# Performance work log

Measured on AMD Instinct MI355X. Metric: run time of the kernel, lower is better.

The kernel has to match this reference:

```python
import jax, jax.numpy as jnp
import numpy as np

TEMPERATURE = 0.07
EPS = 1e-8


def setup_inputs() -> dict:
    key = jax.random.key(0)
    k1, k2 = jax.random.split(key)
    B, D = 8192, 256
    embeddings = jax.random.normal(k1, (B, D), dtype=jnp.float32)
    labels = jax.random.randint(k2, (B,), 0, 6, dtype=jnp.int64)
    return {"embeddings": embeddings, "labels": labels}


def reference(embeddings, labels):
    B = embeddings.shape[0]
    # F.normalize(p=2, dim=1): x / max(||x||, eps)
    norm = jnp.linalg.norm(embeddings, axis=1, keepdims=True)
    en = embeddings / jnp.maximum(norm, 1e-12)
    sim = en @ en.T  # [B, B]
    s = sim / TEMPERATURE

    eye = jnp.eye(B, dtype=bool)
    same = labels[:, None] == labels[None, :]
    pos_mask = same & ~eye            # [B, B]
    neg_mask = (~same) & ~eye         # [B, B]

    exp_s = jnp.exp(s)
    # per-row sum of exp over negatives (matches inner-loop denominator term)
    neg_sum = jnp.sum(jnp.where(neg_mask, exp_s, 0.0), axis=1)  # [B]

    # rows contribute only if they have >=1 positive AND >=1 negative
    row_valid = (pos_mask.sum(axis=1) > 0) & (neg_mask.sum(axis=1) > 0)
    pair_mask = pos_mask & row_valid[:, None]

    # -log( exp(s_ij) / (exp(s_ij) + neg_sum_i + 1e-8) ) per positive pair
    per_pair = -jnp.log(exp_s / (exp_s + neg_sum[:, None] + EPS))
    total = jnp.sum(jnp.where(pair_mask, per_pair, 0.0))
    count = jnp.sum(pair_mask)
    loss = jnp.where(count > 0, total / jnp.maximum(count, 1).astype(total.dtype), 0.0)
    return loss
```

## Files before the change

### kernel.cpp

```cpp
#include <hip/hip_runtime.h>
#include <hip/hip_bf16.h>

#define B_ 8192
#define D_ 256
#define TINV 14.285714285714285f
#define EPS_ 1e-8f
#define BK 32
#define NBLK 32
#define NT 64
#define NTRI (NT*(NT+1)/2)

typedef short short8 __attribute__((ext_vector_type(8)));
typedef float f32x4 __attribute__((ext_vector_type(4)));

__device__ __forceinline__ void mfma_bf16(f32x4& acc, short8 a, short8 b) {
    asm("v_mfma_f32_16x16x32_bf16 %0, %1, %2, %0" : "+v"(acc) : "v"(a), "v"(b));
}

__device__ __forceinline__ void mfma_fence() {
    __builtin_amdgcn_sched_barrier(0);
    asm volatile("s_nop 7\ns_nop 7" ::);
}

__device__ __forceinline__ unsigned short f2bf(float x) {
    __hip_bfloat16 h = __float2bfloat16(x);
    return __builtin_bit_cast(unsigned short, h);
}

__device__ __forceinline__ void tri_decode(int idx, int& bi, int& bj) {
    int t = NTRI - 1 - idx;
    int u = (int)((sqrtf(8.f * (float)t + 1.f) - 1.f) * 0.5f);
    while (u * (u + 1) / 2 > t) --u;
    while ((u + 1) * (u + 2) / 2 <= t) ++u;
    bi = (NT - 1) - u;
    bj = (NT - 1) - (t - u * (u + 1) / 2);
}

__device__ __forceinline__ void stage(const char* gbase, int row0, int k0,
                                      short* ldst, int lane, int wid) {
#pragma unroll
    for (int it = 0; it < 2; ++it) {
        int c = (wid << 1) + it;
        int p = (c << 6) + lane;
        int row = p >> 2;
        int kb = (p & 3) ^ ((row >> 1) & 3);
        const char* g = gbase + ((size_t)(row0 + row) * (D_ * 2) + (size_t)(k0 + kb * 8) * 2);
        __builtin_amdgcn_global_load_lds(
            (const __attribute__((address_space(1))) unsigned int*)g,
            (__attribute__((address_space(3))) unsigned int*)(ldst + (size_t)c * 512),
            16, 0, 0);
    }
}

__device__ __forceinline__ void compute_step(const short* lA, const short* lB,
                                             int lane, int wm, int wn, f32x4 acc[4][4]) {
    int rl = lane & 15, kb = lane >> 4;
    short8 a[4], b[4];
#pragma unroll
    for (int m = 0; m < 4; ++m) {
        int row = wm * 64 + m * 16 + rl;
        a[m] = ((const short8*)lA)[row * 4 + (kb ^ ((row >> 1) & 3))];
    }
#pragma unroll
    for (int n = 0; n < 4; ++n) {
        int row = wn * 64 + n * 16 + rl;
        b[n] = ((const short8*)lB)[row * 4 + (kb ^ ((row >> 1) & 3))];
    }
#pragma unroll
    for (int m = 0; m < 4; ++m)
#pragma unroll
        for (int n = 0; n < 4; ++n)
            mfma_bf16(acc[m][n], a[m], b[n]);
}

__device__ __forceinline__ void gemm_pipe(const char* enb, int i0, int j0,
                                          short (*lA)[128 * BK], short (*lB)[128 * BK],
                                          int lane, int wid, int wm, int wn,
                                          f32x4 acc[4][4]) {
    stage(enb, i0, 0, lA[0], lane, wid);
    stage(enb, j0, 0, lB[0], lane, wid);
#define PIPE_STEP(T, WAITS)                                                     \
    {                                                                           \
        if ((T) < 7) {                                                          \
            stage(enb, i0, ((T) + 1) * BK, lA[((T) + 1) & 1], lane, wid);       \
            stage(enb, j0, ((T) + 1) * BK, lB[((T) + 1) & 1], lane, wid);       \
        }                                                                       \
        asm volatile(WAITS ::: "memory");                                       \
        __builtin_amdgcn_sched_barrier(0);                                      \
        __builtin_amdgcn_s_barrier();                                           \
        __builtin_amdgcn_sched_barrier(0);                                      \
        compute_step(lA[(T) & 1], lB[(T) & 1], lane, wm, wn, acc);              \
        asm volatile("s_waitcnt lgkmcnt(0)" ::: "memory");                      \
        __builtin_amdgcn_sched_barrier(0);                                      \
        __builtin_amdgcn_s_barrier();                                           \
        __builtin_amdgcn_sched_barrier(0);                                      \
    }
    PIPE_STEP(0, "s_waitcnt vmcnt(4)")
    PIPE_STEP(1, "s_waitcnt vmcnt(4)")
    PIPE_STEP(2, "s_waitcnt vmcnt(4)")
    PIPE_STEP(3, "s_waitcnt vmcnt(4)")
    PIPE_STEP(4, "s_waitcnt vmcnt(4)")
    PIPE_STEP(5, "s_waitcnt vmcnt(4)")
    PIPE_STEP(6, "s_waitcnt vmcnt(4)")
    PIPE_STEP(7, "s_waitcnt vmcnt(0)")
#undef PIPE_STEP
    mfma_fence();
}

__global__ __launch_bounds__(256) void k_bhist(const int* __restrict__ labels,
                                               unsigned* __restrict__ blockhist,
                                               float* __restrict__ negsum,
                                               float* __restrict__ total) {
    __shared__ unsigned h[8];
    int b = blockIdx.x, t = threadIdx.x;
    if (t < 8) h[t] = 0;
    negsum[b * 256 + t] = 0.f;
    if (b == 0 && t == 0) *total = 0.f;
    __syncthreads();
    atomicAdd(&h[labels[b * 256 + t] & 7], 1u);
    __syncthreads();
    if (t < 8) blockhist[b * 8 + t] = h[t];
}

__global__ __launch_bounds__(256) void k_pos(const int* __restrict__ labels,
                                             const unsigned* __restrict__ blockhist,
                                             unsigned* __restrict__ hist,
                                             int* __restrict__ pos) {
    __shared__ unsigned cnt[8][NBLK];
    __shared__ unsigned clsbase[8];
    __shared__ unsigned wcnt[4][8];
    int b = blockIdx.x, t = threadIdx.x;
    { int bb = t >> 3, c = t & 7; cnt[c][bb] = blockhist[bb * 8 + c]; }
    __syncthreads();
    if (t < 8) {
        unsigned run = 0;
        for (int b2 = 0; b2 < NBLK; ++b2) {
            unsigned v = cnt[t][b2];
            cnt[t][b2] = run;
            run += v;
        }
        clsbase[t] = run;
        if (b == 0) hist[t] = run;
    }
    __syncthreads();
    if (t == 0) {
        unsigned run = 0;
        for (int c = 0; c < 8; ++c) {
            unsigned tot = clsbase[c];
            clsbase[c] = run;
            run += tot;
        }
    }
    __syncthreads();
    int row = b * 256 + t;
    int c = labels[row] & 7;
    int lane = t & 63, w = t >> 6;
    unsigned long long lanebelow = (1ull << lane) - 1ull;
    unsigned myrank = 0;
#pragma unroll
    for (int cv = 0; cv < 8; ++cv) {
        unsigned long long mask = __ballot(c == cv);
        if (lane == 0) wcnt[w][cv] = (unsigned)__popcll(mask);
        if (c == cv) myrank = (unsigned)__popcll(mask & lanebelow);
    }
    __syncthreads();
    unsigned pre = 0;
    for (int wp = 0; wp < 4; ++wp) if (wp < w) pre += wcnt[wp][c];
    pos[row] = (int)(clsbase[c] + cnt[c][b] + pre + myrank);
}

__global__ __launch_bounds__(256) void k_scatter(const float* __restrict__ emb,
                                                 const int* __restrict__ labels,
                                                 const int* __restrict__ pos,
                                                 __hip_bfloat16* __restrict__ en_s,
                                                 int* __restrict__ lab_s) {
    int row = blockIdx.x * 4 + (threadIdx.x >> 6);
    int lane = threadIdx.x & 63;
    float4 v = reinterpret_cast<const float4*>(emb)[(size_t)row * 64 + lane];
    float ss = v.x * v.x + v.y * v.y + v.z * v.z + v.w * v.w;
#pragma unroll
    for (int off = 32; off >= 1; off >>= 1) ss += __shfl_xor(ss, off, 64);
    float scale = 1.0f / fmaxf(sqrtf(ss), 1e-12f);
    int p = pos[row];
    ushort4 o;
    o.x = f2bf(v.x * scale);
    o.y = f2bf(v.y * scale);
    o.z = f2bf(v.z * scale);
    o.w = f2bf(v.w * scale);
    reinterpret_cast<ushort4*>(en_s)[(size_t)p * 64 + lane] = o;
    if (lane == 0) lab_s[p] = labels[row] & 7;
}

template <bool USEP>
__global__ __launch_bounds__(256) void k_negsum(const __hip_bfloat16* __restrict__ en,
                                                const int* __restrict__ lab_s,
                                                float* __restrict__ P,
                                                float* __restrict__ negsum) {
    __shared__ short lA[2][128 * BK];
    __shared__ short lB[2][128 * BK];
    __shared__ int sLi[128], sLj[128];
    int bi, bj;
    tri_decode(blockIdx.x, bi, bj);
    int i0 = bi * 128, j0 = bj * 128;
    int tid = threadIdx.x;
    if (tid < 128) sLi[tid] = lab_s[i0 + tid];
    else           sLj[tid - 128] = lab_s[j0 + tid - 128];
    __syncthreads();

    int lane = tid & 63, wid = tid >> 6;
    int wm = wid >> 1, wn = wid & 1;
    f32x4 acc[4][4] = {};
    gemm_pipe((const char*)en, i0, j0, lA, lB, lane, wid, wm, wn, acc);

    int rl = lane & 15, rowg = (lane >> 4) * 4;
    int lj[4], li[4][4];
#pragma unroll
    for (int n = 0; n < 4; ++n) lj[n] = sLj[wn * 64 + n * 16 + rl];
#pragma unroll
    for (int m = 0; m < 4; ++m)
#pragma unroll
        for (int r = 0; r < 4; ++r) li[m][r] = sLi[wm * 64 + m * 16 + rowg + r];

#pragma unroll
    for (int m = 0; m < 4; ++m)
#pragma unroll
        for (int n = 0; n < 4; ++n)
#pragma unroll
            for (int r = 0; r < 4; ++r)
                acc[m][n][r] = (li[m][r] != lj[n]) ? __expf(acc[m][n][r] * TINV) : 0.f;

    float* sredR = (float*)lA;
    float* sredC = (float*)lB;

#pragma unroll
    for (int m = 0; m < 4; ++m) {
        float part[4];
#pragma unroll
        for (int r = 0; r < 4; ++r)
            part[r] = acc[m][0][r] + acc[m][1][r] + acc[m][2][r] + acc[m][3][r];
#pragma unroll
        for (int off = 1; off < 16; off <<= 1)
#pragma unroll
            for (int r = 0; r < 4; ++r) part[r] += __shfl_xor(part[r], off, 64);
        if (rl == 0) {
#pragma unroll
            for (int r = 0; r < 4; ++r) {
                int row = wm * 64 + m * 16 + rowg + r;
                if (USEP) sredR[wn * 128 + row] = part[r];
                else      atomicAdd(&negsum[i0 + row], part[r]);
            }
        }
    }
    if (bi != bj) {
#pragma unroll
        for (int n = 0; n < 4; ++n) {
            float cp = 0.f;
#pragma unroll
            for (int m = 0; m < 4; ++m)
#pragma unroll
                for (int r = 0; r < 4; ++r) cp += acc[m][n][r];
            cp += __shfl_xor(cp, 16, 64);
            cp += __shfl_xor(cp, 32, 64);
            if (lane < 16) {
                int col = wn * 64 + n * 16 + rl;
                if (USEP) sredC[wm * 128 + col] = cp;
                else      atomicAdd(&negsum[j0 + col], cp);
            }
        }
    }
    if (USEP) {
        __syncthreads();
        if (tid < 128)
            P[(size_t)bj * B_ + i0 + tid] = sredR[tid] + sredR[128 + tid];
        else if (bi != bj)
            P[(size_t)bi * B_ + j0 + (tid - 128)] = sredC[tid - 128] + sredC[128 + (tid - 128)];
    }
}

__global__ __launch_bounds__(256) void k_red(const float* __restrict__ P,
                                             float* __restrict__ negsum) {
    int i = blockIdx.x * 256 + threadIdx.x;
    float s = 0.f;
#pragma unroll 8
    for (int k = 0; k < 64; ++k) s += P[(size_t)k * B_ + i];
    negsum[i] = s;
}

__global__ __launch_bounds__(256) void k_pairs(const __hip_bfloat16* __restrict__ en,
                                               const int* __restrict__ lab_s,
                                               const float* __restrict__ negsum,
                                               const unsigned* __restrict__ hist,
                                               float* __restrict__ total) {
    int bi, bj;
    tri_decode(blockIdx.x, bi, bj);
    int i0 = bi * 128, j0 = bj * 128;
    if (lab_s[j0] > lab_s[i0 + 127]) return;

    __shared__ short lA[2][128 * BK];
    __shared__ short lB[2][128 * BK];
    __shared__ int sLi[128], sLj[128];
    __shared__ float sNgI[128], sNgJ[128];
    int tid = threadIdx.x;
    if (tid < 128) {
        int l = lab_s[i0 + tid];
        unsigned h = hist[l];
        sLi[tid] = (h > 1u && h < (unsigned)B_) ? l : -1;
        sNgI[tid] = negsum[i0 + tid] + EPS_;
    } else {
        int idx = tid - 128;
        int l = lab_s[j0 + idx];
        unsigned h = hist[l];
        sLj[idx] = (h > 1u && h < (unsigned)B_) ? l : -1;
        sNgJ[idx] = negsum[j0 + idx] + EPS_;
    }
    __syncthreads();

    int lane = tid & 63, wid = tid >> 6;
    int wm = wid >> 1, wn = wid & 1;
    f32x4 acc[4][4] = {};
    gemm_pipe((const char*)en, i0, j0, lA, lB, lane, wid, wm, wn, acc);

    int rl = lane & 15, rowg = (lane >> 4) * 4;
    int lj[4];
    float ngJ[4];
#pragma unroll
    for (int n = 0; n < 4; ++n) {
        lj[n] = sLj[wn * 64 + n * 16 + rl];
        ngJ[n] = sNgJ[wn * 64 + n * 16 + rl];
    }

    bool offd = (bi != bj);
    float tot = 0.f;
#pragma unroll
    for (int m = 0; m < 4; ++m) {
#pragma unroll
        for (int r = 0; r < 4; ++r) {
            int ii = wm * 64 + m * 16 + rowg + r;
            int li = sLi[ii];
            float ngI = sNgI[ii];
#pragma unroll
            for (int n = 0; n < 4; ++n) {
                int jj = wn * 64 + n * 16 + rl;
                bool use = (li == lj[n]) && (li >= 0) && (offd || ii != jj);
                if (use) {
                    float s = acc[m][n][r] * TINV;
                    float e = __expf(s);
                    float t = __logf(e + ngI) - s;
                    if (offd) t += __logf(e + ngJ[n]) - s;
                    tot += t;
                }
            }
        }
    }
#pragma unroll
    for (int off = 32; off >= 1; off >>= 1) tot += __shfl_xor(tot, off, 64);
    __shared__ float sred[4];
    if (lane == 0) sred[wid] = tot;
    __syncthreads();
    if (tid == 0) atomicAdd(total, sred[0] + sred[1] + sred[2] + sred[3]);
}

__global__ __launch_bounds__(64) void k_final(const unsigned* __restrict__ hist,
                                              const float* __restrict__ total,
                                              float* __restrict__ out) {
    int t = threadIdx.x;
    unsigned c = 0;
    if (t < 8) {
        unsigned h = hist[t];
        if (h > 1u && h < (unsigned)B_) c = h * (h - 1u);
    }
#pragma unroll
    for (int off = 4; off >= 1; off >>= 1) c += (unsigned)__shfl_xor((int)c, off, 64);
    if (t == 0) out[0] = (c > 0u) ? total[0] / (float)c : 0.f;
}

extern "C" void kernel_launch(void* const* d_in, const int* in_sizes, int n_in,
                              void* d_out, int out_size, void* d_ws, size_t ws_size,
                              hipStream_t stream) {
    const float* emb = (const float*)d_in[0];
    const int* labels = (const int*)d_in[1];
    float* out = (float*)d_out;
    char* ws = (char*)d_ws;

    const size_t EN_BYTES = (size_t)B_ * D_ * 2;
    __hip_bfloat16* en_s = (__hip_bfloat16*)ws;
    char* p = ws + EN_BYTES;
    float* negsum = (float*)p;            p += (size_t)B_ * 4;
    int* lab_s = (int*)p;                 p += (size_t)B_ * 4;
    int* pos = (int*)p;                   p += (size_t)B_ * 4;
    unsigned* blockhist = (unsigned*)p;   p += NBLK * 8 * 4;
    unsigned* hist = (unsigned*)p;        p += 64;
    float* total = (float*)p;             p += 64;
    float* P = (float*)p;
    size_t need = (size_t)(p - ws) + (size_t)NT * B_ * 4;
    bool bigws = ws_size >= need;

    k_bhist<<<NBLK, 256, 0, stream>>>(labels, blockhist, negsum, total);
    k_pos<<<NBLK, 256, 0, stream>>>(labels, blockhist, hist, pos);
    k_scatter<<<B_ / 4, 256, 0, stream>>>(emb, labels, pos, en_s, lab_s);
    if (bigws) {
        k_negsum<true><<<NTRI, 256, 0, stream>>>(en_s, lab_s, P, negsum);
        k_red<<<B_ / 256, 256, 0, stream>>>(P, negsum);
    } else {
        k_negsum<false><<<NTRI, 256, 0, stream>>>(en_s, lab_s, P, negsum);
    }
    k_pairs<<<NTRI, 256, 0, stream>>>(en_s, lab_s, negsum, hist, total);
    k_final<<<1, 64, 0, stream>>>(hist, total, out);
}
```

Measured before the change: 78.02 us.

## Enlarge GEMM tiles to 256x256 with 512-thread blocks and BK=64 pipeline

Both k_negsum and k_pairs now use 256x256 output tiles with 8 waves (each owning a 128x64 sub-tile) and BK=64 K-steps with an 8-chunk XOR swizzle. This cuts the triangular grid from 2080 to 528 blocks and halves the K-loop iterations, so each block reuses more data per load and spends less on barriers. The MFMA bursts are wrapped in s_setprio, and the negsum exp and row-reduction are fused into one pass. In exchange, more registers and LDS are used per block, and fewer blocks may leave CUs underfilled and hurt load balance across the triangle.

```diff
diff --git a/kernel.cpp b/kernel.cpp
--- a/kernel.cpp
+++ b/kernel.cpp
@@ -5,9 +5,9 @@
 #define D_ 256
 #define TINV 14.285714285714285f
 #define EPS_ 1e-8f
-#define BK 32
+#define BK 64
 #define NBLK 32
-#define NT 64
+#define NT 32
 #define NTRI (NT*(NT+1)/2)
 
 typedef short short8 __attribute__((ext_vector_type(8)));
@@ -39,71 +39,74 @@
 __device__ __forceinline__ void stage(const char* gbase, int row0, int k0,
                                       short* ldst, int lane, int wid) {
 #pragma unroll
-    for (int it = 0; it < 2; ++it) {
-        int c = (wid << 1) + it;
-        int p = (c << 6) + lane;
-        int row = p >> 2;
-        int kb = (p & 3) ^ ((row >> 1) & 3);
-        const char* g = gbase + ((size_t)(row0 + row) * (D_ * 2) + (size_t)(k0 + kb * 8) * 2);
+    for (int it = 0; it < 4; ++it) {
+        int sb = ((it << 3) + wid) << 6;
+        int p = sb + lane;
+        int row = p >> 3;
+        int c = (p & 7) ^ (row & 7);
+        const char* g = gbase + ((size_t)(row0 + row) * (D_ * 2) + (size_t)(k0 + (c << 3)) * 2);
         __builtin_amdgcn_global_load_lds(
             (const __attribute__((address_space(1))) unsigned int*)g,
-            (__attribute__((address_space(3))) unsigned int*)(ldst + (size_t)c * 512),
+            (__attribute__((address_space(3))) unsigned int*)(ldst + ((size_t)sb << 3)),
             16, 0, 0);
     }
 }
 
-__device__ __forceinline__ void compute_step(const short* lA, const short* lB,
-                                             int lane, int wm, int wn, f32x4 acc[4][4]) {
-    int rl = lane & 15, kb = lane >> 4;
-    short8 a[4], b[4];
-#pragma unroll
-    for (int m = 0; m < 4; ++m) {
-        int row = wm * 64 + m * 16 + rl;
-        a[m] = ((const short8*)lA)[row * 4 + (kb ^ ((row >> 1) & 3))];
-    }
-#pragma unroll
-    for (int n = 0; n < 4; ++n) {
-        int row = wn * 64 + n * 16 + rl;
-        b[n] = ((const short8*)lB)[row * 4 + (kb ^ ((row >> 1) & 3))];
-    }
-#pragma unroll
-    for (int m = 0; m < 4; ++m)
-#pragma unroll
-        for (int n = 0; n < 4; ++n)
-            mfma_bf16(acc[m][n], a[m], b[n]);
-}
+__device__ __forceinline__ void compute_tile(const short* lA, const short* lB,
+                                             int lane, int wm, int wn, f32x4 acc[8][4]) {
+    int rl = lane & 15, kq = lane >> 4;
+#pragma unroll
+    for (int kk = 0; kk < 2; ++kk) {
+        int c = (kk << 2) + kq;
+        short8 a[8], b[4];
+#pragma unroll
+        for (int m = 0; m < 8; ++m) {
+            int row = wm * 128 + m * 16 + rl;
+            a[m] = ((const short8*)lA)[row * 8 + (c ^ (row & 7))];
+        }
+#pragma unroll
+        for (int n = 0; n < 4; ++n) {
+            int row = wn * 64 + n * 16 + rl;
+            b[n] = ((const short8*)lB)[row * 8 + (c ^ (row & 7))];
+        }
+        __builtin_amdgcn_s_setprio(1);
+#pragma unroll
+        for (int m = 0; m < 8; ++m)
+#pragma unroll
+            for (int n = 0; n < 4; ++n)
+                mfma_bf16(acc[m][n], a[m], b[n]);
+        __builtin_amdgcn_s_setprio(0);
+    }
+}
+
+#define WBAR(W)                                     \
+    asm volatile(W ::: "memory");                   \
+    __builtin_amdgcn_sched_barrier(0);              \
+    __builtin_amdgcn_s_barrier();                   \
+    __builtin_amdgcn_sched_barrier(0);
 
 __device__ __forceinline__ void gemm_pipe(const char* enb, int i0, int j0,
-                                          short (*lA)[128 * BK], short (*lB)[128 * BK],
+                                          short (*lA)[256 * BK], short (*lB)[256 * BK],
                                           int lane, int wid, int wm, int wn,
-                                          f32x4 acc[4][4]) {
+                                          f32x4 acc[8][4]) {
     stage(enb, i0, 0, lA[0], lane, wid);
     stage(enb, j0, 0, lB[0], lane, wid);
-#define PIPE_STEP(T, WAITS)                                                     \
-    {                                                                           \
-        if ((T) < 7) {                                                          \
-            stage(enb, i0, ((T) + 1) * BK, lA[((T) + 1) & 1], lane, wid);       \
-            stage(enb, j0, ((T) + 1) * BK, lB[((T) + 1) & 1], lane, wid);       \
-        }                                                                       \
-        asm volatile(WAITS ::: "memory");                                       \
-        __builtin_amdgcn_sched_barrier(0);                                      \
-        __builtin_amdgcn_s_barrier();                                           \
-        __builtin_amdgcn_sched_barrier(0);                                      \
-        compute_step(lA[(T) & 1], lB[(T) & 1], lane, wm, wn, acc);              \
-        asm volatile("s_waitcnt lgkmcnt(0)" ::: "memory");                      \
-        __builtin_amdgcn_sched_barrier(0);                                      \
-        __builtin_amdgcn_s_barrier();                                           \
-        __builtin_amdgcn_sched_barrier(0);                                      \
-    }
-    PIPE_STEP(0, "s_waitcnt vmcnt(4)")
-    PIPE_STEP(1, "s_waitcnt vmcnt(4)")
-    PIPE_STEP(2, "s_waitcnt vmcnt(4)")
-    PIPE_STEP(3, "s_waitcnt vmcnt(4)")
-    PIPE_STEP(4, "s_waitcnt vmcnt(4)")
-    PIPE_STEP(5, "s_waitcnt vmcnt(4)")
-    PIPE_STEP(6, "s_waitcnt vmcnt(4)")
-    PIPE_STEP(7, "s_waitcnt vmcnt(0)")
-#undef PIPE_STEP
+    stage(enb, i0, BK, lA[1], lane, wid);
+    stage(enb, j0, BK, lB[1], lane, wid);
+    WBAR("s_waitcnt vmcnt(8)")
+    compute_tile(lA[0], lB[0], lane, wm, wn, acc);
+    WBAR("s_waitcnt lgkmcnt(0)")
+    stage(enb, i0, 2 * BK, lA[0], lane, wid);
+    stage(enb, j0, 2 * BK, lB[0], lane, wid);
+    WBAR("s_waitcnt vmcnt(8)")
+    compute_tile(lA[1], lB[1], lane, wm, wn, acc);
+    WBAR("s_waitcnt lgkmcnt(0)")
+    stage(enb, i0, 3 * BK, lA[1], lane, wid);
+    stage(enb, j0, 3 * BK, lB[1], lane, wid);
+    WBAR("s_waitcnt vmcnt(8)")
+    compute_tile(lA[0], lB[0], lane, wm, wn, acc);
+    WBAR("s_waitcnt vmcnt(0)")
+    compute_tile(lA[1], lB[1], lane, wm, wn, acc);
     mfma_fence();
 }
 
@@ -192,52 +195,50 @@
 }
 
 template <bool USEP>
-__global__ __launch_bounds__(256) void k_negsum(const __hip_bfloat16* __restrict__ en,
-                                                const int* __restrict__ lab_s,
-                                                float* __restrict__ P,
-                                                float* __restrict__ negsum) {
-    __shared__ short lA[2][128 * BK];
-    __shared__ short lB[2][128 * BK];
-    __shared__ int sLi[128], sLj[128];
+__global__ __launch_bounds__(512, 2) void k_negsum(const __hip_bfloat16* __restrict__ en,
+                                                   const int* __restrict__ lab_s,
+                                                   float* __restrict__ P,
+                                                   float* __restrict__ negsum) {
+    __shared__ short lA[2][256 * BK];
+    __shared__ short lB[2][256 * BK];
+    __shared__ int sLi[256], sLj[256];
     int bi, bj;
     tri_decode(blockIdx.x, bi, bj);
-    int i0 = bi * 128, j0 = bj * 128;
+    int i0 = bi * 256, j0 = bj * 256;
     int tid = threadIdx.x;
-    if (tid < 128) sLi[tid] = lab_s[i0 + tid];
-    else           sLj[tid - 128] = lab_s[j0 + tid - 128];
+    if (tid < 256) sLi[tid] = lab_s[i0 + tid];
+    else           sLj[tid - 256] = lab_s[j0 + tid - 256];
     __syncthreads();
 
     int lane = tid & 63, wid = tid >> 6;
-    int wm = wid >> 1, wn = wid & 1;
-    f32x4 acc[4][4] = {};
+    int wm = wid >> 2, wn = wid & 3;
+    f32x4 acc[8][4] = {};
     gemm_pipe((const char*)en, i0, j0, lA, lB, lane, wid, wm, wn, acc);
 
-    int rl = lane & 15, rowg = (lane >> 4) * 4;
-    int lj[4], li[4][4];
+    int rl = lane & 15, rowg = (lane >> 4) << 2;
+    int lj[4];
 #pragma unroll
     for (int n = 0; n < 4; ++n) lj[n] = sLj[wn * 64 + n * 16 + rl];
-#pragma unroll
-    for (int m = 0; m < 4; ++m)
-#pragma unroll
-        for (int r = 0; r < 4; ++r) li[m][r] = sLi[wm * 64 + m * 16 + rowg + r];
-
-#pragma unroll
-    for (int m = 0; m < 4; ++m)
+
+    float* sredR = (float*)lA;
+    float* sredC = (float*)lA + 2048;
+
+#pragma unroll
+    for (int m = 0; m < 8; ++m) {
+        int lir[4]; float part[4];
+#pragma unroll
+        for (int r = 0; r < 4; ++r) {
+            lir[r] = sLi[wm * 128 + m * 16 + rowg + r];
+            part[r] = 0.f;
+        }
 #pragma unroll
         for (int n = 0; n < 4; ++n)
 #pragma unroll
-            for (int r = 0; r < 4; ++r)
-                acc[m][n][r] = (li[m][r] != lj[n]) ? __expf(acc[m][n][r] * TINV) : 0.f;
-
-    float* sredR = (float*)lA;
-    float* sredC = (float*)lB;
-
-#pragma unroll
-    for (int m = 0; m < 4; ++m) {
-        float part[4];
-#pragma unroll
-        for (int r = 0; r < 4; ++r)
-            part[r] = acc[m][0][r] + acc[m][1][r] + acc[m][2][r] + acc[m][3][r];
+            for (int r = 0; r < 4; ++r) {
+                float e = (lir[r] != lj[n]) ? __expf(acc[m][n][r] * TINV) : 0.f;
+                acc[m][n][r] = e;
+                part[r] += e;
+            }
 #pragma unroll
         for (int off = 1; off < 16; off <<= 1)
 #pragma unroll
@@ -245,9 +246,9 @@
         if (rl == 0) {
 #pragma unroll
             for (int r = 0; r < 4; ++r) {
-                int row = wm * 64 + m * 16 + rowg + r;
-                if (USEP) sredR[wn * 128 + row] = part[r];
-                else      atomicAdd(&negsum[i0 + row], part[r]);
+                int rr = m * 16 + rowg + r;
+                if (USEP) sredR[(wm * 4 + wn) * 128 + rr] = part[r];
+                else      atomicAdd(&negsum[i0 + wm * 128 + rr], part[r]);
             }
         }
     }
@@ -256,24 +257,29 @@
         for (int n = 0; n < 4; ++n) {
             float cp = 0.f;
 #pragma unroll
-            for (int m = 0; m < 4; ++m)
+            for (int m = 0; m < 8; ++m)
 #pragma unroll
                 for (int r = 0; r < 4; ++r) cp += acc[m][n][r];
             cp += __shfl_xor(cp, 16, 64);
             cp += __shfl_xor(cp, 32, 64);
             if (lane < 16) {
                 int col = wn * 64 + n * 16 + rl;
-                if (USEP) sredC[wm * 128 + col] = cp;
+                if (USEP) sredC[wm * 256 + col] = cp;
                 else      atomicAdd(&negsum[j0 + col], cp);
             }
         }
     }
     if (USEP) {
         __syncthreads();
-        if (tid < 128)
-            P[(size_t)bj * B_ + i0 + tid] = sredR[tid] + sredR[128 + tid];
-        else if (bi != bj)
-            P[(size_t)bi * B_ + j0 + (tid - 128)] = sredC[tid - 128] + sredC[128 + (tid - 128)];
+        if (tid < 256) {
+            int wmh = tid >> 7, rr = tid & 127;
+            float s = sredR[(wmh * 4 + 0) * 128 + rr] + sredR[(wmh * 4 + 1) * 128 + rr]
+                    + sredR[(wmh * 4 + 2) * 128 + rr] + sredR[(wmh * 4 + 3) * 128 + rr];
+            P[(size_t)bj * B_ + i0 + tid] = s;
+        } else if (bi != bj) {
+            int c2 = tid - 256;
+            P[(size_t)bi * B_ + j0 + c2] = sredC[c2] + sredC[256 + c2];
+        }
     }
 }
 
@@ -282,32 +288,32 @@
     int i = blockIdx.x * 256 + threadIdx.x;
     float s = 0.f;
 #pragma unroll 8
-    for (int k = 0; k < 64; ++k) s += P[(size_t)k * B_ + i];
+    for (int k = 0; k < NT; ++k) s += P[(size_t)k * B_ + i];
     negsum[i] = s;
 }
 
-__global__ __launch_bounds__(256) void k_pairs(const __hip_bfloat16* __restrict__ en,
-                                               const int* __restrict__ lab_s,
-                                               const float* __restrict__ negsum,
-                                               const unsigned* __restrict__ hist,
-                                               float* __restrict__ total) {
+__global__ __launch_bounds__(512, 2) void k_pairs(const __hip_bfloat16* __restrict__ en,
+                                                  const int* __restrict__ lab_s,
+                                                  const float* __restrict__ negsum,
+                                                  const unsigned* __restrict__ hist,
+                                                  float* __restrict__ total) {
     int bi, bj;
     tri_decode(blockIdx.x, bi, bj);
-    int i0 = bi * 128, j0 = bj * 128;
-    if (lab_s[j0] > lab_s[i0 + 127]) return;
-
-    __shared__ short lA[2][128 * BK];
-    __shared__ short lB[2][128 * BK];
-    __shared__ int sLi[128], sLj[128];
-    __shared__ float sNgI[128], sNgJ[128];
+    int i0 = bi * 256, j0 = bj * 256;
+    if (lab_s[j0] > lab_s[i0 + 255]) return;
+
+    __shared__ short lA[2][256 * BK];
+    __shared__ short lB[2][256 * BK];
+    __shared__ int sLi[256], sLj[256];
+    __shared__ float sNgI[256], sNgJ[256];
     int tid = threadIdx.x;
-    if (tid < 128) {
+    if (tid < 256) {
         int l = lab_s[i0 + tid];
         unsigned h = hist[l];
         sLi[tid] = (h > 1u && h < (unsigned)B_) ? l : -1;
         sNgI[tid] = negsum[i0 + tid] + EPS_;
     } else {
-        int idx = tid - 128;
+        int idx = tid - 256;
         int l = lab_s[j0 + idx];
         unsigned h = hist[l];
         sLj[idx] = (h > 1u && h < (unsigned)B_) ? l : -1;
@@ -316,11 +322,11 @@
     __syncthreads();
 
     int lane = tid & 63, wid = tid >> 6;
-    int wm = wid >> 1, wn = wid & 1;
-    f32x4 acc[4][4] = {};
+    int wm = wid >> 2, wn = wid & 3;
+    f32x4 acc[8][4] = {};
     gemm_pipe((const char*)en, i0, j0, lA, lB, lane, wid, wm, wn, acc);
 
-    int rl = lane & 15, rowg = (lane >> 4) * 4;
+    int rl = lane & 15, rowg = (lane >> 4) << 2;
     int lj[4];
     float ngJ[4];
 #pragma unroll
@@ -332,10 +338,10 @@
     bool offd = (bi != bj);
     float tot = 0.f;
 #pragma unroll
-    for (int m = 0; m < 4; ++m) {
+    for (int m = 0; m < 8; ++m) {
 #pragma unroll
         for (int r = 0; r < 4; ++r) {
-            int ii = wm * 64 + m * 16 + rowg + r;
+            int ii = wm * 128 + m * 16 + rowg + r;
             int li = sLi[ii];
             float ngI = sNgI[ii];
 #pragma unroll
@@ -354,10 +360,15 @@
     }
 #pragma unroll
     for (int off = 32; off >= 1; off >>= 1) tot += __shfl_xor(tot, off, 64);
-    __shared__ float sred[4];
+    float* sred = (float*)lA;
     if (lane == 0) sred[wid] = tot;
     __syncthreads();
-    if (tid == 0) atomicAdd(total, sred[0] + sred[1] + sred[2] + sred[3]);
+    if (tid == 0) {
+        float s = 0.f;
+#pragma unroll
+        for (int w = 0; w < 8; ++w) s += sred[w];
+        atomicAdd(total, s);
+    }
 }
 
 __global__ __launch_bounds__(64) void k_final(const unsigned* __restrict__ hist,
@@ -399,11 +410,11 @@
     k_pos<<<NBLK, 256, 0, stream>>>(labels, blockhist, hist, pos);
     k_scatter<<<B_ / 4, 256, 0, stream>>>(emb, labels, pos, en_s, lab_s);
     if (bigws) {
-        k_negsum<true><<<NTRI, 256, 0, stream>>>(en_s, lab_s, P, negsum);
+        k_negsum<true><<<NTRI, 512, 0, stream>>>(en_s, lab_s, P, negsum);
         k_red<<<B_ / 256, 256, 0, stream>>>(P, negsum);
     } else {
-        k_negsum<false><<<NTRI, 256, 0, stream>>>(en_s, lab_s, P, negsum);
-    }
-    k_pairs<<<NTRI, 256, 0, stream>>>(en_s, lab_s, negsum, hist, total);
+        k_negsum<false><<<NTRI, 512, 0, stream>>>(en_s, lab_s, P, negsum);
+    }
+    k_pairs<<<NTRI, 512, 0, stream>>>(en_s, lab_s, negsum, hist, total);
     k_final<<<1, 64, 0, stream>>>(hist, total, out);
 }
```

Result: slower. 92.19 us (+18.2%).
